# Kernel tuning notes

Measured on AMD Instinct MI355X. Metric: run time of the kernel, lower is better.

Reference implementation:

```python
import jax, jax.numpy as jnp
import numpy as np
from jax import lax

EPS = 1e-5

def _bn(x, g, b, m, v):
    # inference batchnorm over channel axis 1 of NCHW
    s = g / jnp.sqrt(v + EPS)
    return x * s[None, :, None, None] + (b - m * s)[None, :, None, None]

def _conv1x1(x, w, b):
    # x: [B,C,H,W], w: [O,C]
    return jnp.einsum('bchw,oc->bohw', x, w) + b[None, :, None, None]

def _dwconv3(x, w, b):
    # depthwise 3x3, stride 1, pad 1; w: [C,1,3,3]
    y = lax.conv_general_dilated(x, w, (1, 1), ((1, 1), (1, 1)),
                                 dimension_numbers=('NCHW', 'OIHW', 'NCHW'),
                                 feature_group_count=x.shape[1])
    return y + b[None, :, None, None]

def _frelu(x, dw, db, dg, dbb, dm, dv):
    return jnp.maximum(x, _bn(_dwconv3(x, dw, db), dg, dbb, dm, dv))

def _branch(x, cw, cb, bg, bb, bm, bv, dw, db, dg, dbb, dm, dv):
    # Conv1x1 -> BN -> FReLU
    y = _bn(_conv1x1(x, cw, cb), bg, bb, bm, bv)
    return _frelu(y, dw, db, dg, dbb, dm, dv)

def setup_inputs() -> dict:
    key = jax.random.key(0)
    ks = jax.random.split(key, 30)
    B, C, H, W = 8, 512, 64, 64
    Kc, Vc, O = 256, 256, 512
    f32 = jnp.float32
    def rn(k, shape, s):
        return jax.random.normal(k, shape, f32) * s
    def rp(k, shape):
        return jax.random.uniform(k, shape, f32, 0.5, 1.5)
    inp = {
        'x': rn(ks[0], (B, C, H, W), 1.0),
        # f_key branch
        'fk_cw': rn(ks[1], (Kc, C), C ** -0.5), 'fk_cb': rn(ks[2], (Kc,), 0.02),
        'fk_bg': rp(ks[3], (Kc,)), 'fk_bb': rn(ks[4], (Kc,), 0.02),
        'fk_bm': rn(ks[5], (Kc,), 0.1), 'fk_bv': rp(ks[6], (Kc,)),
        'fk_dw': rn(ks[7], (Kc, 1, 3, 3), 1.0 / 3.0), 'fk_db': rn(ks[8], (Kc,), 0.02),
        'fk_dg': rp(ks[9], (Kc,)), 'fk_dbb': rn(ks[10], (Kc,), 0.02),
        'fk_dm': rn(ks[11], (Kc,), 0.1), 'fk_dv': rp(ks[12], (Kc,)),
        # f_value branch (also used as f_query)
        'fv_cw': rn(ks[13], (Vc, C), C ** -0.5), 'fv_cb': rn(ks[14], (Vc,), 0.02),
        'fv_bg': rp(ks[15], (Vc,)), 'fv_bb': rn(ks[16], (Vc,), 0.02),
        'fv_bm': rn(ks[17], (Vc,), 0.1), 'fv_bv': rp(ks[18], (Vc,)),
        'fv_dw': rn(ks[19], (Vc, 1, 3, 3), 1.0 / 3.0), 'fv_db': rn(ks[20], (Vc,), 0.02),
        'fv_dg': rp(ks[21], (Vc,)), 'fv_dbb': rn(ks[22], (Vc,), 0.02),
        'fv_dm': rn(ks[23], (Vc,), 0.1), 'fv_dv': rp(ks[24], (Vc,)),
        # output projection W (zero-init in source; randomized here for testing)
        'w_w': rn(ks[25], (O, Kc), Kc ** -0.5), 'w_b': rn(ks[26], (O,), 0.02),
    }
    return inp

def reference(x, fk_cw, fk_cb, fk_bg, fk_bb, fk_bm, fk_bv, fk_dw, fk_db, fk_dg, fk_dbb, fk_dm, fk_dv,
              fv_cw, fv_cb, fv_bg, fv_bb, fv_bm, fv_bv, fv_dw, fv_db, fv_dg, fv_dbb, fv_dm, fv_dv,
              w_w, w_b):
    B, C, H, W = x.shape
    N = H * W
    kf = _branch(x, fk_cw, fk_cb, fk_bg, fk_bb, fk_bm, fk_bv, fk_dw, fk_db, fk_dg, fk_dbb, fk_dm, fk_dv)  # [B,Kc,H,W]
    vf = _branch(x, fv_cw, fv_cb, fv_bg, fv_bb, fv_bm, fv_bv, fv_dw, fv_db, fv_dg, fv_dbb, fv_dm, fv_dv)  # [B,Vc,H,W]
    query = vf.reshape(B, -1, N)              # [B,Vc,N] (f_query aliases f_value)
    value = query.transpose(0, 2, 1)          # [B,N,Vc]
    key_t = kf.reshape(B, -1, N).transpose(0, 2, 1)  # [B,N,Kc]
    # NOTE: faithful to source -- similarity is channel-wise [Vc,Kc], not spatial NxN
    sim = jnp.einsum('bvn,bnk->bvk', query, key_t) * (float(N) ** -0.5)
    sim = jax.nn.softmax(sim, axis=-1)        # softmax over Kc
    ctx = jnp.einsum('bnv,bvk->bnk', value, sim)     # [B,N,Kc]
    ctx = ctx.transpose(0, 2, 1).reshape(B, -1, H, W)  # [B,Kc,H,W]
    return _conv1x1(ctx, w_w, w_b)            # [B,O,H,W]
```

## Files before the change

kernel.cpp:

```cpp
#include <hip/hip_runtime.h>
#include <stdint.h>

typedef __bf16 bf16;
typedef __bf16 bf16x8 __attribute__((ext_vector_type(8)));
typedef __bf16 bf16x4 __attribute__((ext_vector_type(4)));
typedef float f32x4 __attribute__((ext_vector_type(4)));
typedef unsigned short u16x8 __attribute__((ext_vector_type(8)));

#define B_    8
#define C_    512
#define N_    4096
#define OC2_  512
#define KC_   256

typedef __attribute__((address_space(1))) const uint32_t* gas1_t;
typedef __attribute__((address_space(3))) uint32_t* las3_t;

__device__ __forceinline__ void gload16(const void* g, void* l) {
  __builtin_amdgcn_global_load_lds((gas1_t)g, (las3_t)l, 16, 0, 0);
}

__global__ __launch_bounds__(256) void prep_kernel(
    const float* __restrict__ fk_cw, const float* __restrict__ fk_cb,
    const float* __restrict__ fk_bg, const float* __restrict__ fk_bb,
    const float* __restrict__ fk_bm, const float* __restrict__ fk_bv,
    const float* __restrict__ fk_dw, const float* __restrict__ fk_db,
    const float* __restrict__ fk_dg, const float* __restrict__ fk_dbb,
    const float* __restrict__ fk_dm, const float* __restrict__ fk_dv,
    const float* __restrict__ fv_cw, const float* __restrict__ fv_cb,
    const float* __restrict__ fv_bg, const float* __restrict__ fv_bb,
    const float* __restrict__ fv_bm, const float* __restrict__ fv_bv,
    const float* __restrict__ fv_dw, const float* __restrict__ fv_db,
    const float* __restrict__ fv_dg, const float* __restrict__ fv_dbb,
    const float* __restrict__ fv_dm, const float* __restrict__ fv_dv,
    const float* __restrict__ w_w,
    bf16* __restrict__ Wcat, bf16* __restrict__ Ww,
    float* __restrict__ sconv, float* __restrict__ tconv,
    float* __restrict__ wdw9, float* __restrict__ tdw)
{
  int i = blockIdx.x * 256 + threadIdx.x;
  if (i < 262144) {
    int oc = i >> 9, c = i & 511;
    float v = (oc < 256) ? fk_cw[oc * 512 + c] : fv_cw[(oc - 256) * 512 + c];
    Wcat[i] = (bf16)v;
  } else if (i < 393216) {
    int j = i - 262144;
    Ww[j] = (bf16)w_w[j];
  } else if (i < 393728) {
    int oc = i - 393216;
    float g, bb, m, v, cb;
    if (oc < 256) { g = fk_bg[oc]; bb = fk_bb[oc]; m = fk_bm[oc]; v = fk_bv[oc]; cb = fk_cb[oc]; }
    else { int c2 = oc - 256; g = fv_bg[c2]; bb = fv_bb[c2]; m = fv_bm[c2]; v = fv_bv[c2]; cb = fv_cb[c2]; }
    float s = g / sqrtf(v + 1e-5f);
    sconv[oc] = s;
    tconv[oc] = cb * s + bb - m * s;
  } else if (i < 394240) {
    int oc = i - 393728;
    float g, bb, m, v, db;
    const float* dwp;
    if (oc < 256) { g = fk_dg[oc]; bb = fk_dbb[oc]; m = fk_dm[oc]; v = fk_dv[oc]; db = fk_db[oc]; dwp = fk_dw + oc * 9; }
    else { int c2 = oc - 256; g = fv_dg[c2]; bb = fv_dbb[c2]; m = fv_dm[c2]; v = fv_dv[c2]; db = fv_db[c2]; dwp = fv_dw + c2 * 9; }
    float s2 = g / sqrtf(v + 1e-5f);
    for (int j = 0; j < 9; ++j) wdw9[oc * 9 + j] = dwp[j] * s2;
    tdw[oc] = db * s2 + bb - m * s2;
  }
}

__global__ __launch_bounds__(256) void k0_transpose(const float* __restrict__ x,
                                                    bf16* __restrict__ xb)
{
  __shared__ float t[64 * 64];
  int nt = blockIdx.x, ct = blockIdx.y, b = blockIdx.z;
  int tid = threadIdx.x;
  const float* src = x + ((size_t)(b * C_ + ct * 64)) * N_ + nt * 64;
#pragma unroll
  for (int i = 0; i < 4; ++i) {
    int chunk = tid + i * 256;
    int c = chunk >> 4, c4 = chunk & 15;
    float4 v = *(const float4*)(src + (size_t)c * N_ + c4 * 4);
    int n0 = c4 * 4, k = c & 31;
    t[c * 64 + ((n0 + 0) ^ k)] = v.x;
    t[c * 64 + ((n0 + 1) ^ k)] = v.y;
    t[c * 64 + ((n0 + 2) ^ k)] = v.z;
    t[c * 64 + ((n0 + 3) ^ k)] = v.w;
  }
  __syncthreads();
  bf16* dst = xb + ((size_t)b * N_ + nt * 64) * C_ + ct * 64;
#pragma unroll
  for (int i = 0; i < 2; ++i) {
    int u = tid + i * 256;
    int nl = u >> 3, c8 = u & 7;
    bf16x8 o;
#pragma unroll
    for (int j = 0; j < 8; ++j) {
      int cc = c8 * 8 + j;
      o[j] = (bf16)t[cc * 64 + (nl ^ (cc & 31))];
    }
    *(bf16x8*)(dst + (size_t)nl * C_ + c8 * 8) = o;
  }
}

template<int EPI, int MTILES, int NTILES, int KSPLIT, int KCHUNK>
__global__ __launch_bounds__(256, 2) void gemm_tn(
    const bf16* __restrict__ A, int lda, size_t sA,
    const bf16* __restrict__ Bm, int ldb, size_t sB,
    void* __restrict__ Cv, int ldc, size_t sC,
    const float* __restrict__ e0, const float* __restrict__ e1)
{
  __shared__ bf16 As[128 * 64];
  __shared__ bf16 Bs[128 * 64];
  int bid = blockIdx.x;
  int ks  = bid % KSPLIT; bid /= KSPLIT;
  int ntl = bid % NTILES; bid /= NTILES;
  int mtl = bid % MTILES; bid /= MTILES;
  int b = bid;
  const bf16* Ab = A  + (size_t)b * sA + (size_t)mtl * 128 * lda + ks * KCHUNK;
  const bf16* Bb = Bm + (size_t)b * sB + (size_t)ntl * 128 * ldb + ks * KCHUNK;
  int tid = threadIdx.x;
  int lane = tid & 63, w = tid >> 6;
  int mb = (w >> 1) * 64, nb = (w & 1) * 64;
  int lrow = lane & 15, lk = (lane >> 4) * 8;

  f32x4 acc[4][4];
#pragma unroll
  for (int i = 0; i < 4; ++i)
#pragma unroll
    for (int j = 0; j < 4; ++j) acc[i][j] = 0.f;

  for (int kt = 0; kt < KCHUNK / 64; ++kt) {
    __syncthreads();
#pragma unroll
    for (int i = 0; i < 4; ++i) {
      int chunk = tid + i * 256;
      int row = chunk >> 3, c8 = chunk & 7;
      gload16(Ab + (size_t)row * lda + kt * 64 + c8 * 8, &As[chunk * 8]);
      gload16(Bb + (size_t)row * ldb + kt * 64 + c8 * 8, &Bs[chunk * 8]);
    }
    __syncthreads();
#pragma unroll
    for (int kk = 0; kk < 2; ++kk) {
      bf16x8 af[4], bfr[4];
#pragma unroll
      for (int mi = 0; mi < 4; ++mi)
        af[mi] = *reinterpret_cast<const bf16x8*>(&As[(mb + mi * 16 + lrow) * 64 + kk * 32 + lk]);
#pragma unroll
      for (int ni = 0; ni < 4; ++ni)
        bfr[ni] = *reinterpret_cast<const bf16x8*>(&Bs[(nb + ni * 16 + lrow) * 64 + kk * 32 + lk]);
#pragma unroll
      for (int mi = 0; mi < 4; ++mi)
#pragma unroll
        for (int ni = 0; ni < 4; ++ni)
          acc[mi][ni] = __builtin_amdgcn_mfma_f32_16x16x32_bf16(af[mi], bfr[ni], acc[mi][ni], 0, 0, 0);
    }
  }

  int col = lane & 15, r0 = (lane >> 4) * 4;
#pragma unroll
  for (int mi = 0; mi < 4; ++mi) {
#pragma unroll
    for (int ni = 0; ni < 4; ++ni) {
#pragma unroll
      for (int r = 0; r < 4; ++r) {
        int gm = mtl * 128 + mb + mi * 16 + r0 + r;
        int gn = ntl * 128 + nb + ni * 16 + col;
        float v = acc[mi][ni][r];
        size_t o = (size_t)b * sC + (size_t)gm * ldc + gn;
        if constexpr (EPI == 0)      ((bf16*)Cv)[o] = (bf16)(v * e0[gm] + e1[gm]);
        else if constexpr (EPI == 1) atomicAdd(&((float*)Cv)[o], v * 0.015625f);
        else if constexpr (EPI == 2) ((bf16*)Cv)[o] = (bf16)v;
        else                         ((float*)Cv)[o] = v + e0[gm];
      }
    }
  }
}

__global__ __launch_bounds__(256) void k2_dwfrelu(
    const bf16* __restrict__ y, const float* __restrict__ wdw9,
    const float* __restrict__ tdw, bf16* __restrict__ kf, bf16* __restrict__ vfc)
{
  __shared__ bf16 pl[66 * 66];
  int ch = blockIdx.x, b = blockIdx.y;
  int tid = threadIdx.x;
  if (tid < 66) { pl[tid] = (bf16)0.f; pl[65 * 66 + tid] = (bf16)0.f; }
  const bf16* src = y + ((size_t)(b * OC2_ + ch)) * N_;
#pragma unroll
  for (int i = 0; i < 2; ++i) {
    int u = tid + i * 256;
    int r = u >> 3, c8 = u & 7;
    uint4 d = *(const uint4*)(src + (size_t)r * 64 + c8 * 8);
    uint32_t* lp = (uint32_t*)&pl[(r + 1) * 66 + c8 * 8];
    lp[0] = d.x; lp[1] = d.y; lp[2] = d.z; lp[3] = d.w;
  }
  __syncthreads();
  float wf[9];
#pragma unroll
  for (int j = 0; j < 9; ++j) wf[j] = wdw9[ch * 9 + j];
  float tb = tdw[ch];
  int r = tid >> 2, ws0 = (tid & 3) * 16;
  float row0[18], row1[18], row2[18];
#pragma unroll
  for (int j = 0; j < 18; ++j) {
    int c = ws0 + j - 1;
    bool ok = (c >= 0) && (c < 64);
    row0[j] = ok ? (float)pl[(r + 0) * 66 + c] : 0.f;
    row1[j] = ok ? (float)pl[(r + 1) * 66 + c] : 0.f;
    row2[j] = ok ? (float)pl[(r + 2) * 66 + c] : 0.f;
  }
  bf16x8 o0, o1;
#pragma unroll
  for (int wi = 0; wi < 16; ++wi) {
    float a = row0[wi] * wf[0] + row0[wi + 1] * wf[1] + row0[wi + 2] * wf[2]
            + row1[wi] * wf[3] + row1[wi + 1] * wf[4] + row1[wi + 2] * wf[5]
            + row2[wi] * wf[6] + row2[wi + 1] * wf[7] + row2[wi + 2] * wf[8] + tb;
    float z = fmaxf(row1[wi + 1], a);
    if (wi < 8) o0[wi] = (bf16)z; else o1[wi - 8] = (bf16)z;
  }
  bf16* dst = (ch < KC_) ? (kf + ((size_t)(b * KC_ + ch)) * N_)
                         : (vfc + ((size_t)(b * KC_ + ch - KC_)) * N_);
  *(bf16x8*)(dst + (size_t)r * 64 + ws0) = o0;
  *(bf16x8*)(dst + (size_t)r * 64 + ws0 + 8) = o1;
}

__global__ __launch_bounds__(256) void k2b_transpose(const bf16* __restrict__ vfc,
                                                     bf16* __restrict__ vfh)
{
  __shared__ uint32_t t[64 * 64];
  int nt = blockIdx.x, vt = blockIdx.y, b = blockIdx.z;
  int tid = threadIdx.x;
  const uint16_t* src = (const uint16_t*)(vfc + ((size_t)(b * KC_ + vt * 64)) * N_ + nt * 64);
#pragma unroll
  for (int i = 0; i < 2; ++i) {
    int u = tid + i * 256;
    int v = u >> 3, c8 = u & 7;
    u16x8 d = *(const u16x8*)(src + (size_t)v * N_ + c8 * 8);
#pragma unroll
    for (int j = 0; j < 8; ++j) {
      int n = c8 * 8 + j;
      t[v * 64 + (n ^ (v & 31))] = d[j];
    }
  }
  __syncthreads();
  uint16_t* dst = (uint16_t*)(vfh + ((size_t)b * N_ + nt * 64) * KC_ + vt * 64);
#pragma unroll
  for (int i = 0; i < 2; ++i) {
    int u = tid + i * 256;
    int nl = u >> 3, v8 = u & 7;
    u16x8 o;
#pragma unroll
    for (int j = 0; j < 8; ++j) {
      int v = v8 * 8 + j;
      o[j] = (uint16_t)t[v * 64 + (nl ^ (v & 31))];
    }
    *(u16x8*)(dst + (size_t)nl * KC_ + v8 * 8) = o;
  }
}

__global__ __launch_bounds__(256) void softmax_k(const float* __restrict__ sim,
                                                 bf16* __restrict__ P)
{
  int row = blockIdx.x * 4 + (threadIdx.x >> 6);
  int lane = threadIdx.x & 63;
  float4 v = ((const float4*)(sim + (size_t)row * 256))[lane];
  float mx = fmaxf(fmaxf(v.x, v.y), fmaxf(v.z, v.w));
#pragma unroll
  for (int s = 32; s; s >>= 1) mx = fmaxf(mx, __shfl_xor(mx, s));
  float a0 = __expf(v.x - mx), a1 = __expf(v.y - mx);
  float a2 = __expf(v.z - mx), a3 = __expf(v.w - mx);
  float sm = a0 + a1 + a2 + a3;
#pragma unroll
  for (int s = 32; s; s >>= 1) sm += __shfl_xor(sm, s);
  float inv = 1.0f / sm;
  bf16x4 o;
  o[0] = (bf16)(a0 * inv); o[1] = (bf16)(a1 * inv);
  o[2] = (bf16)(a2 * inv); o[3] = (bf16)(a3 * inv);
  *(bf16x4*)(P + (size_t)row * 256 + lane * 4) = o;
}

extern "C" void kernel_launch(void* const* d_in, const int* in_sizes, int n_in,
                              void* d_out, int out_size, void* d_ws, size_t ws_size,
                              hipStream_t stream) {
  const float* x      = (const float*)d_in[0];
  const float* fk_cw  = (const float*)d_in[1];
  const float* fk_cb  = (const float*)d_in[2];
  const float* fk_bg  = (const float*)d_in[3];
  const float* fk_bb  = (const float*)d_in[4];
  const float* fk_bm  = (const float*)d_in[5];
  const float* fk_bv  = (const float*)d_in[6];
  const float* fk_dw  = (const float*)d_in[7];
  const float* fk_db  = (const float*)d_in[8];
  const float* fk_dg  = (const float*)d_in[9];
  const float* fk_dbb = (const float*)d_in[10];
  const float* fk_dm  = (const float*)d_in[11];
  const float* fk_dv  = (const float*)d_in[12];
  const float* fv_cw  = (const float*)d_in[13];
  const float* fv_cb  = (const float*)d_in[14];
  const float* fv_bg  = (const float*)d_in[15];
  const float* fv_bb  = (const float*)d_in[16];
  const float* fv_bm  = (const float*)d_in[17];
  const float* fv_bv  = (const float*)d_in[18];
  const float* fv_dw  = (const float*)d_in[19];
  const float* fv_db  = (const float*)d_in[20];
  const float* fv_dg  = (const float*)d_in[21];
  const float* fv_dbb = (const float*)d_in[22];
  const float* fv_dm  = (const float*)d_in[23];
  const float* fv_dv  = (const float*)d_in[24];
  const float* w_w    = (const float*)d_in[25];
  const float* w_b    = (const float*)d_in[26];

  char* wsp = (char*)d_ws;
  size_t off = 0;
  auto take = [&](size_t bytes) -> void* {
    void* p = wsp + off;
    off += (bytes + 255) & ~(size_t)255;
    return p;
  };
  bf16*  xb    = (bf16*) take((size_t)B_ * N_ * C_ * 2);
  bf16*  y     = (bf16*) take((size_t)B_ * OC2_ * N_ * 2);
  bf16*  kf    = (bf16*) take((size_t)B_ * KC_ * N_ * 2);
  bf16*  vfc   = (bf16*) take((size_t)B_ * KC_ * N_ * 2);
  float* sim   = (float*)take((size_t)B_ * KC_ * KC_ * 4);
  bf16*  P     = (bf16*) take((size_t)B_ * KC_ * KC_ * 2);
  bf16*  MmT   = (bf16*) take((size_t)B_ * 512 * KC_ * 2);
  bf16*  Wcat  = (bf16*) take((size_t)512 * 512 * 2);
  bf16*  Ww    = (bf16*) take((size_t)512 * 256 * 2);
  float* sconv = (float*)take(512 * 4);
  float* tconv = (float*)take(512 * 4);
  float* wdw9  = (float*)take(512 * 9 * 4);
  float* tdwb  = (float*)take(512 * 4);
  bf16*  vfh   = xb;

  prep_kernel<<<1540, 256, 0, stream>>>(
      fk_cw, fk_cb, fk_bg, fk_bb, fk_bm, fk_bv, fk_dw, fk_db, fk_dg, fk_dbb, fk_dm, fk_dv,
      fv_cw, fv_cb, fv_bg, fv_bb, fv_bm, fv_bv, fv_dw, fv_db, fv_dg, fv_dbb, fv_dm, fv_dv,
      w_w, Wcat, Ww, sconv, tconv, wdw9, tdwb);

  k0_transpose<<<dim3(64, 8, 8), 256, 0, stream>>>(x, xb);

  gemm_tn<0, 4, 32, 1, 512><<<dim3(1024), 256, 0, stream>>>(
      Wcat, 512, 0, xb, 512, (size_t)N_ * C_, y, 4096, (size_t)OC2_ * N_, sconv, tconv);

  k2_dwfrelu<<<dim3(512, 8), 256, 0, stream>>>(y, wdw9, tdwb, kf, vfc);
  k2b_transpose<<<dim3(64, 4, 8), 256, 0, stream>>>(vfc, vfh);

  hipMemsetAsync(sim, 0, (size_t)B_ * KC_ * KC_ * 4, stream);
  gemm_tn<1, 2, 2, 8, 512><<<dim3(256), 256, 0, stream>>>(
      vfc, 4096, (size_t)KC_ * N_, kf, 4096, (size_t)KC_ * N_,
      sim, 256, (size_t)KC_ * KC_, nullptr, nullptr);

  softmax_k<<<dim3(512), 256, 0, stream>>>(sim, P);

  gemm_tn<2, 4, 2, 1, 256><<<dim3(64), 256, 0, stream>>>(
      Ww, 256, 0, P, 256, (size_t)KC_ * KC_,
      MmT, 256, (size_t)512 * KC_, nullptr, nullptr);

  gemm_tn<3, 4, 32, 1, 256><<<dim3(1024), 256, 0, stream>>>(
      MmT, 256, (size_t)512 * KC_, vfh, 256, (size_t)N_ * KC_,
      (float*)d_out, 4096, (size_t)512 * N_, w_b, nullptr);
}
```

Before: 265.7 us.

## Replace split-K atomics with partial buffers reduced in softmax; vectorize dwconv LDS reads

The similarity GEMM no longer zeroes the output with a memset and accumulates split-K partials through float atomics. Each K-split now writes its own partial slice, and the softmax kernel sums the 8 slices before normalising. Separately, the depthwise 3x3 kernel pads each LDS row to 72 elements so that it can read the row window with 16-byte vector loads instead of scalar element loads. The cost is an 8x larger sim scratch buffer and extra reads in softmax, which together add about 16MB of traffic.

```diff
diff --git a/kernel.cpp b/kernel.cpp
--- a/kernel.cpp
+++ b/kernel.cpp
@@ -164,11 +164,14 @@
         int gm = mtl * 128 + mb + mi * 16 + r0 + r;
         int gn = ntl * 128 + nb + ni * 16 + col;
         float v = acc[mi][ni][r];
-        size_t o = (size_t)b * sC + (size_t)gm * ldc + gn;
-        if constexpr (EPI == 0)      ((bf16*)Cv)[o] = (bf16)(v * e0[gm] + e1[gm]);
-        else if constexpr (EPI == 1) atomicAdd(&((float*)Cv)[o], v * 0.015625f);
-        else if constexpr (EPI == 2) ((bf16*)Cv)[o] = (bf16)v;
-        else                         ((float*)Cv)[o] = v + e0[gm];
+        if constexpr (EPI == 4) {
+          ((float*)Cv)[((size_t)b * KSPLIT + ks) * sC + (size_t)gm * ldc + gn] = v * 0.015625f;
+        } else {
+          size_t o = (size_t)b * sC + (size_t)gm * ldc + gn;
+          if constexpr (EPI == 0)      ((bf16*)Cv)[o] = (bf16)(v * e0[gm] + e1[gm]);
+          else if constexpr (EPI == 2) ((bf16*)Cv)[o] = (bf16)v;
+          else                         ((float*)Cv)[o] = v + e0[gm];
+        }
       }
     }
   }
@@ -178,17 +181,17 @@
     const bf16* __restrict__ y, const float* __restrict__ wdw9,
     const float* __restrict__ tdw, bf16* __restrict__ kf, bf16* __restrict__ vfc)
 {
-  __shared__ bf16 pl[66 * 66];
+  __shared__ bf16 pl[66 * 72];
   int ch = blockIdx.x, b = blockIdx.y;
   int tid = threadIdx.x;
-  if (tid < 66) { pl[tid] = (bf16)0.f; pl[65 * 66 + tid] = (bf16)0.f; }
+  if (tid < 72) { pl[tid] = (bf16)0.f; pl[65 * 72 + tid] = (bf16)0.f; }
   const bf16* src = y + ((size_t)(b * OC2_ + ch)) * N_;
 #pragma unroll
   for (int i = 0; i < 2; ++i) {
     int u = tid + i * 256;
     int r = u >> 3, c8 = u & 7;
     uint4 d = *(const uint4*)(src + (size_t)r * 64 + c8 * 8);
-    uint32_t* lp = (uint32_t*)&pl[(r + 1) * 66 + c8 * 8];
+    uint32_t* lp = (uint32_t*)&pl[(r + 1) * 72 + c8 * 8];
     lp[0] = d.x; lp[1] = d.y; lp[2] = d.z; lp[3] = d.w;
   }
   __syncthreads();
@@ -197,22 +200,24 @@
   for (int j = 0; j < 9; ++j) wf[j] = wdw9[ch * 9 + j];
   float tb = tdw[ch];
   int r = tid >> 2, ws0 = (tid & 3) * 16;
-  float row0[18], row1[18], row2[18];
-#pragma unroll
-  for (int j = 0; j < 18; ++j) {
-    int c = ws0 + j - 1;
-    bool ok = (c >= 0) && (c < 64);
-    row0[j] = ok ? (float)pl[(r + 0) * 66 + c] : 0.f;
-    row1[j] = ok ? (float)pl[(r + 1) * 66 + c] : 0.f;
-    row2[j] = ok ? (float)pl[(r + 2) * 66 + c] : 0.f;
+  float win[3][18];
+#pragma unroll
+  for (int row = 0; row < 3; ++row) {
+    const bf16* rp = &pl[(r + row) * 72];
+    bf16x8 v0 = *reinterpret_cast<const bf16x8*>(rp + ws0);
+    bf16x8 v1 = *reinterpret_cast<const bf16x8*>(rp + ws0 + 8);
+    win[row][0]  = (ws0 > 0)  ? (float)rp[ws0 - 1]  : 0.f;
+    win[row][17] = (ws0 < 48) ? (float)rp[ws0 + 16] : 0.f;
+#pragma unroll
+    for (int j = 0; j < 8; ++j) { win[row][1 + j] = (float)v0[j]; win[row][9 + j] = (float)v1[j]; }
   }
   bf16x8 o0, o1;
 #pragma unroll
   for (int wi = 0; wi < 16; ++wi) {
-    float a = row0[wi] * wf[0] + row0[wi + 1] * wf[1] + row0[wi + 2] * wf[2]
-            + row1[wi] * wf[3] + row1[wi + 1] * wf[4] + row1[wi + 2] * wf[5]
-            + row2[wi] * wf[6] + row2[wi + 1] * wf[7] + row2[wi + 2] * wf[8] + tb;
-    float z = fmaxf(row1[wi + 1], a);
+    float a = win[0][wi] * wf[0] + win[0][wi + 1] * wf[1] + win[0][wi + 2] * wf[2]
+            + win[1][wi] * wf[3] + win[1][wi + 1] * wf[4] + win[1][wi + 2] * wf[5]
+            + win[2][wi] * wf[6] + win[2][wi + 1] * wf[7] + win[2][wi + 2] * wf[8] + tb;
+    float z = fmaxf(win[1][wi + 1], a);
     if (wi < 8) o0[wi] = (bf16)z; else o1[wi - 8] = (bf16)z;
   }
   bf16* dst = (ch < KC_) ? (kf + ((size_t)(b * KC_ + ch)) * N_)
@@ -255,20 +260,25 @@
   }
 }
 
-__global__ __launch_bounds__(256) void softmax_k(const float* __restrict__ sim,
+__global__ __launch_bounds__(256) void softmax_k(const float* __restrict__ simp,
                                                  bf16* __restrict__ P)
 {
   int row = blockIdx.x * 4 + (threadIdx.x >> 6);
+  int b = row >> 8, v = row & 255;
   int lane = threadIdx.x & 63;
-  float4 v = ((const float4*)(sim + (size_t)row * 256))[lane];
-  float mx = fmaxf(fmaxf(v.x, v.y), fmaxf(v.z, v.w));
-#pragma unroll
-  for (int s = 32; s; s >>= 1) mx = fmaxf(mx, __shfl_xor(mx, s));
-  float a0 = __expf(v.x - mx), a1 = __expf(v.y - mx);
-  float a2 = __expf(v.z - mx), a3 = __expf(v.w - mx);
+  const float* base = simp + (size_t)b * 8 * 65536 + (size_t)v * 256 + lane * 4;
+  f32x4 s = 0.f;
+#pragma unroll
+  for (int ks = 0; ks < 8; ++ks)
+    s += *reinterpret_cast<const f32x4*>(base + (size_t)ks * 65536);
+  float mx = fmaxf(fmaxf(s[0], s[1]), fmaxf(s[2], s[3]));
+#pragma unroll
+  for (int sh = 32; sh; sh >>= 1) mx = fmaxf(mx, __shfl_xor(mx, sh));
+  float a0 = __expf(s[0] - mx), a1 = __expf(s[1] - mx);
+  float a2 = __expf(s[2] - mx), a3 = __expf(s[3] - mx);
   float sm = a0 + a1 + a2 + a3;
 #pragma unroll
-  for (int s = 32; s; s >>= 1) sm += __shfl_xor(sm, s);
+  for (int sh = 32; sh; sh >>= 1) sm += __shfl_xor(sm, sh);
   float inv = 1.0f / sm;
   bf16x4 o;
   o[0] = (bf16)(a0 * inv); o[1] = (bf16)(a1 * inv);
@@ -318,7 +328,7 @@
   bf16*  y     = (bf16*) take((size_t)B_ * OC2_ * N_ * 2);
   bf16*  kf    = (bf16*) take((size_t)B_ * KC_ * N_ * 2);
   bf16*  vfc   = (bf16*) take((size_t)B_ * KC_ * N_ * 2);
-  float* sim   = (float*)take((size_t)B_ * KC_ * KC_ * 4);
+  float* simp  = (float*)take((size_t)B_ * 8 * 65536 * 4);
   bf16*  P     = (bf16*) take((size_t)B_ * KC_ * KC_ * 2);
   bf16*  MmT   = (bf16*) take((size_t)B_ * 512 * KC_ * 2);
   bf16*  Wcat  = (bf16*) take((size_t)512 * 512 * 2);
@@ -342,12 +352,11 @@
   k2_dwfrelu<<<dim3(512, 8), 256, 0, stream>>>(y, wdw9, tdwb, kf, vfc);
   k2b_transpose<<<dim3(64, 4, 8), 256, 0, stream>>>(vfc, vfh);
 
-  hipMemsetAsync(sim, 0, (size_t)B_ * KC_ * KC_ * 4, stream);
-  gemm_tn<1, 2, 2, 8, 512><<<dim3(256), 256, 0, stream>>>(
+  gemm_tn<4, 2, 2, 8, 512><<<dim3(256), 256, 0, stream>>>(
       vfc, 4096, (size_t)KC_ * N_, kf, 4096, (size_t)KC_ * N_,
-      sim, 256, (size_t)KC_ * KC_, nullptr, nullptr);
-
-  softmax_k<<<dim3(512), 256, 0, stream>>>(sim, P);
+      simp, 256, 65536, nullptr, nullptr);
+
+  softmax_k<<<dim3(512), 256, 0, stream>>>(simp, P);
 
   gemm_tn<2, 4, 2, 1, 256><<<dim3(64), 256, 0, stream>>>(
       Ww, 256, 0, P, 256, (size_t)KC_ * KC_,
```

After: 262.7 us. Within noise of the previous version (-1.2%).
